# Performance work log

Measured on AMD Instinct MI355X. Metric: run time of the kernel, lower is better.

Reference implementation:

```python
import jax, jax.numpy as jnp
import numpy as np
from jax import lax

D_MODEL = 512
CLASS_NUM = 8000
MAX_LEN = 80
VOCAB = 8002  # len(char2idx): chars + sos/eos
SOS_IDX = 0


def setup_inputs() -> dict:
    key = jax.random.key(0)
    ks = jax.random.split(key, 16)
    T, B, D, V, C = 128, 128, D_MODEL, VOCAB, CLASS_NUM
    s = 1.0 / np.sqrt(D)
    inp = {
        "inputs": jax.random.normal(ks[0], (T, B, D), jnp.float32),
        # additive attention params (query_size=key_size=hidden_size=D)
        "Wq": jax.random.normal(ks[1], (D, D), jnp.float32) * s,
        "bq": jnp.zeros((D,), jnp.float32),
        "Wk": jax.random.normal(ks[2], (D, D), jnp.float32) * s,
        "bk": jnp.zeros((D,), jnp.float32),
        "v": jax.random.normal(ks[3], (D,), jnp.float32) * s,
        # GRUCell: input_size = 2*D, hidden_size = D (PyTorch layout)
        "W_ih": jax.random.normal(ks[4], (3 * D, 2 * D), jnp.float32) * s,
        "b_ih": jnp.zeros((3 * D,), jnp.float32),
        "W_hh": jax.random.normal(ks[5], (3 * D, D), jnp.float32) * s,
        "b_hh": jnp.zeros((3 * D,), jnp.float32),
        # embedding table and classifier
        "emb": jax.random.normal(ks[6], (V, D), jnp.float32),
        "Wc": jax.random.normal(ks[7], (C, D), jnp.float32) * s,
        "bc": jnp.zeros((C,), jnp.float32),
    }
    return inp


def _gru_cell(x, h, W_ih, b_ih, W_hh, b_hh):
    # PyTorch GRUCell math
    gi = x @ W_ih.T + b_ih  # [B, 3D]
    gh = h @ W_hh.T + b_hh  # [B, 3D]
    i_r, i_z, i_n = jnp.split(gi, 3, axis=1)
    h_r, h_z, h_n = jnp.split(gh, 3, axis=1)
    r = jax.nn.sigmoid(i_r + h_r)
    z = jax.nn.sigmoid(i_z + h_z)
    n = jnp.tanh(i_n + r * h_n)
    return (1.0 - z) * n + z * h


def reference(inputs, Wq, bq, Wk, bk, v, W_ih, b_ih, W_hh, b_hh, emb, Wc, bc):
    T, B, D = inputs.shape
    # Attention is called as attention(inputs, keys) with keys = inputs each
    # step -> weights are loop-invariant; compute the context once.
    e = jnp.tanh(inputs @ Wq.T + bq + inputs @ Wk.T + bk) @ v  # [T, B]
    att = jax.nn.softmax(e, axis=0)[..., None]  # [T, B, 1]
    c = jnp.sum(att * inputs, axis=0)  # [B, D]

    h0 = inputs[0]  # initial GRU hidden = first encoder frame
    out0 = emb[jnp.full((B,), SOS_IDX, dtype=jnp.int32)]  # sos embedding

    def step(carry, _):
        h, out = carry
        x = jnp.concatenate([out, c], axis=1)  # [B, 2D]
        h = _gru_cell(x, h, W_ih, b_ih, W_hh, b_hh)
        pred = h @ Wc.T + bc  # [B, class_num]
        top1 = jnp.argmax(pred, axis=1)  # greedy decode (eval mode)
        return (h, emb[top1]), pred

    _, preds = lax.scan(step, (h0, out0), None, length=MAX_LEN)
    return preds  # [max_len, B, class_num]
```

## Files before the change

### kernel.cpp

```cpp
#include <hip/hip_runtime.h>
#include <cstdint>
#include <cstddef>

#define D_MOD 512
#define TH3   1536
#define CLS   8000
#define MAXLEN 80
#define B_SZ  128
#define T_LEN 128
#define NK0   16
#define EGI_ROWS 8000

typedef __attribute__((ext_vector_type(8))) __bf16 bf16x8;
typedef __attribute__((ext_vector_type(8))) unsigned short u16x8;
typedef __attribute__((ext_vector_type(4))) float f32x4;

__device__ __forceinline__ unsigned short f2bf(float x) {
    unsigned u = __float_as_uint(x);
    unsigned r = ((u >> 16) & 1u) + 0x7fffu;
    return (unsigned short)((u + r) >> 16);
}
__device__ __forceinline__ float bf2f(unsigned short h) {
    return __uint_as_float(((unsigned)h) << 16);
}
__device__ __forceinline__ f32x4 mfma16(u16x8 a, u16x8 b, f32x4 c) {
    return __builtin_amdgcn_mfma_f32_16x16x32_bf16(
        __builtin_bit_cast(bf16x8, a), __builtin_bit_cast(bf16x8, b), c, 0, 0, 0);
}
__device__ __forceinline__ void conv8(const float* __restrict__ p, u16x8& hi, u16x8& lo) {
    float4 f0 = *(const float4*)p;
    float4 f1 = *(const float4*)(p + 4);
    float fs[8] = {f0.x, f0.y, f0.z, f0.w, f1.x, f1.y, f1.z, f1.w};
    #pragma unroll
    for (int j = 0; j < 8; ++j) {
        unsigned short h = f2bf(fs[j]);
        hi[j] = h;
        lo[j] = f2bf(fs[j] - bf2f(h));
    }
}
__device__ __forceinline__ unsigned long long packkey(float v, int n) {
    unsigned u = __float_as_uint(v);
    u = (u & 0x80000000u) ? ~u : (u | 0x80000000u);
    return ((unsigned long long)u << 32) | (unsigned)(~(unsigned)n);
}
__device__ __forceinline__ unsigned long long shfl_xor_u64(unsigned long long x, int mask) {
    unsigned lo = (unsigned)x, hi = (unsigned)(x >> 32);
    lo = __shfl_xor(lo, mask, 16);
    hi = __shfl_xor(hi, mask, 16);
    return ((unsigned long long)hi << 32) | lo;
}
__device__ __forceinline__ size_t pk_off(int n, int k) {
    int tile = n >> 4, lr = n & 15, k0i = k >> 5, lk = (k >> 3) & 3, e = k & 7;
    return ((size_t)(tile * NK0 + k0i) * 64 + (lk * 16 + lr)) * 8 + e;
}

__global__ __launch_bounds__(256) void cvt2p_kernel(
    const float* __restrict__ s1, const float* __restrict__ s2, int ld,
    long total4, unsigned short* __restrict__ hi, unsigned short* __restrict__ lo)
{
    long i4 = (long)blockIdx.x * 256 + threadIdx.x;
    if (i4 >= total4) return;
    long r = i4 >> 7;
    int c = (int)(i4 & 127) * 4;
    float4 a = *(const float4*)(s1 + r * (long)ld + c);
    if (s2) {
        float4 b = *(const float4*)(s2 + r * (long)ld + c);
        a.x += b.x; a.y += b.y; a.z += b.z; a.w += b.w;
    }
    float xs[4] = {a.x, a.y, a.z, a.w};
    unsigned short hs[4], ls[4];
    #pragma unroll
    for (int j = 0; j < 4; ++j) {
        hs[j] = f2bf(xs[j]);
        ls[j] = f2bf(xs[j] - bf2f(hs[j]));
    }
    size_t o = pk_off((int)r, c);
    *(ushort4*)(hi + o) = make_ushort4(hs[0], hs[1], hs[2], hs[3]);
    *(ushort4*)(lo + o) = make_ushort4(ls[0], ls[1], ls[2], ls[3]);
}

template<bool GATHER_CONV, bool CONVB, bool ADD2D, bool ARGMAX, int NS, int KS>
__device__ __forceinline__ void gemm_ks2(
    float* __restrict__ red,
    const unsigned short* __restrict__ Ahi, const unsigned short* __restrict__ Alo,
    const float* __restrict__ Afp, const unsigned long long* __restrict__ gslot,
    const unsigned short* __restrict__ Bhi, const unsigned short* __restrict__ Blo,
    const float* __restrict__ Bfp,
    const float* __restrict__ bias, const float* __restrict__ D2,
    float* __restrict__ C, int ldc,
    unsigned long long* __restrict__ aslot, int bx, int by)
{
    static_assert(NS * KS == 8, "8 waves per block");
    const int tid = threadIdx.x;
    const int w = tid >> 6, lane = tid & 63;
    const int lr = lane & 15, lk = lane >> 4;
    const int ns = w % NS, ks = w / NS;
    const int m0 = by * 16;
    const int n0 = (bx * NS + ns) * 32;
    const int tA = by;
    const int tB0 = n0 >> 4, tB1 = tB0 + 1;

    const float* paf = nullptr;
    if constexpr (GATHER_CONV) {
        int g = gslot ? (int)(~(unsigned)gslot[m0 + lr]) : (m0 + lr);
        paf = Afp + (size_t)g * D_MOD + lk * 8;
    }
    const float *pb0f = nullptr, *pb1f = nullptr;
    if constexpr (CONVB) {
        pb0f = Bfp + (size_t)(n0 + lr) * D_MOD + lk * 8;
        pb1f = Bfp + (size_t)(n0 + 16 + lr) * D_MOD + lk * 8;
    }

    f32x4 acc0 = (f32x4){0.f, 0.f, 0.f, 0.f};
    f32x4 acc1 = (f32x4){0.f, 0.f, 0.f, 0.f};

    const int kBeg = ks * (NK0 / KS), kEnd = kBeg + (NK0 / KS);
    for (int k0i = kBeg; k0i < kEnd; ++k0i) {
        u16x8 ah, al, b0h, b0l, b1h, b1l;
        if constexpr (GATHER_CONV) {
            conv8(paf + k0i * 32, ah, al);
        } else {
            size_t oA = ((size_t)(tA * NK0 + k0i) * 64 + lane) * 8;
            ah = *(const u16x8*)(Ahi + oA); al = *(const u16x8*)(Alo + oA);
        }
        if constexpr (CONVB) {
            conv8(pb0f + k0i * 32, b0h, b0l);
            conv8(pb1f + k0i * 32, b1h, b1l);
        } else {
            size_t oB0 = ((size_t)(tB0 * NK0 + k0i) * 64 + lane) * 8;
            size_t oB1 = ((size_t)(tB1 * NK0 + k0i) * 64 + lane) * 8;
            b0h = *(const u16x8*)(Bhi + oB0); b0l = *(const u16x8*)(Blo + oB0);
            b1h = *(const u16x8*)(Bhi + oB1); b1l = *(const u16x8*)(Blo + oB1);
        }
        acc0 = mfma16(ah, b0h, acc0);
        acc0 = mfma16(ah, b0l, acc0);
        acc0 = mfma16(al, b0h, acc0);
        acc1 = mfma16(ah, b1h, acc1);
        acc1 = mfma16(ah, b1l, acc1);
        acc1 = mfma16(al, b1h, acc1);
    }

    float af[8];
    #pragma unroll
    for (int i = 0; i < 4; ++i) { af[i] = acc0[i]; af[4 + i] = acc1[i]; }

    if (ks > 0) {
        const int slot = (ks - 1) * NS + ns;
        #pragma unroll
        for (int i = 0; i < 8; ++i) red[slot * 576 + lane * 9 + i] = af[i];
    }
    __syncthreads();
    if (ks == 0) {
        #pragma unroll
        for (int j = 1; j < KS; ++j) {
            const int slot = (j - 1) * NS + ns;
            #pragma unroll
            for (int i = 0; i < 8; ++i) af[i] += red[slot * 576 + lane * 9 + i];
        }
        #pragma unroll
        for (int r = 0; r < 4; ++r) {
            const int row = m0 + lk * 4 + r;
            unsigned long long kmax = 0ull;
            #pragma unroll
            for (int ni = 0; ni < 2; ++ni) {
                const int col = n0 + ni * 16 + lr;
                float val = af[ni * 4 + r];
                if (bias) val += bias[col];
                if constexpr (ADD2D) val += D2[(size_t)row * ldc + col];
                C[(size_t)row * ldc + col] = val;
                if constexpr (ARGMAX) {
                    unsigned long long k = packkey(val, col);
                    if (k > kmax) kmax = k;
                }
            }
            if constexpr (ARGMAX) {
                #pragma unroll
                for (int off = 1; off < 16; off <<= 1) {
                    unsigned long long o = shfl_xor_u64(kmax, off);
                    if (o > kmax) kmax = o;
                }
                if (lr == 0) atomicMax(&aslot[row], kmax);
            }
        }
    }
}

template<int G>
__device__ __forceinline__ bool xcd_map(int p, int& bx, int& by) {
    int x = p & 7, s = p >> 3;
    by = s & 7;
    bx = x * G + (s >> 3);
    return true;
}

__global__ __launch_bounds__(512) void egi_kernel(
    const float* __restrict__ emb,
    const unsigned short* __restrict__ WihaHi, const unsigned short* __restrict__ WihaLo,
    float* __restrict__ Egi)
{
    __shared__ float red[7 * 576];
    int p = blockIdx.x;
    int x = p & 7, s = p >> 3;
    int by = s % 500, bx = x * 6 + s / 500;
    gemm_ks2<true, false, false, false, 1, 8>(red, nullptr, nullptr, emb, nullptr,
        WihaHi, WihaLo, nullptr, nullptr, nullptr, Egi, TH3, nullptr, bx, by);
}

__global__ __launch_bounds__(512) void gh_kernel(
    const unsigned short* __restrict__ hHi, const unsigned short* __restrict__ hLo,
    const unsigned short* __restrict__ WhhHi, const unsigned short* __restrict__ WhhLo,
    const float* __restrict__ b_hh, float* __restrict__ gh)
{
    __shared__ float red[7 * 576];
    int bx, by;
    xcd_map<6>(blockIdx.x, bx, by);
    gemm_ks2<false, false, false, false, 1, 8>(red, hHi, hLo, nullptr, nullptr,
        WhhHi, WhhLo, nullptr, b_hh, nullptr, gh, TH3, nullptr, bx, by);
}

template<bool CONVB>
__global__ __launch_bounds__(512) void cls_gh_kernel(
    const unsigned short* __restrict__ hHi, const unsigned short* __restrict__ hLo,
    const unsigned short* __restrict__ WcHi, const unsigned short* __restrict__ WcLo,
    const float* __restrict__ Wc, const float* __restrict__ bc,
    float* __restrict__ C, unsigned long long* __restrict__ aslot,
    const unsigned short* __restrict__ WhhHi, const unsigned short* __restrict__ WhhLo,
    const float* __restrict__ b_hh, float* __restrict__ gh)
{
    __shared__ float red[7 * 576];
    const int p = blockIdx.x;
    if (p < 1024) {
        int bx, by;
        xcd_map<16>(p, bx, by);
        if (bx >= 125) return;
        gemm_ks2<false, CONVB, false, true, 2, 4>(red, hHi, hLo, nullptr, nullptr,
            WcHi, WcLo, Wc, bc, nullptr, C, CLS, aslot, bx, by);
    } else {
        int bx, by;
        xcd_map<6>(p - 1024, bx, by);
        gemm_ks2<false, false, false, false, 1, 8>(red, hHi, hLo, nullptr, nullptr,
            WhhHi, WhhLo, nullptr, b_hh, nullptr, gh, TH3, nullptr, bx, by);
    }
}

__global__ __launch_bounds__(512) void step_dual_kernel(
    const unsigned short* __restrict__ hHi, const unsigned short* __restrict__ hLo,
    const unsigned short* __restrict__ WhhHi, const unsigned short* __restrict__ WhhLo,
    const float* __restrict__ b_hh,
    const float* __restrict__ emb, const unsigned long long* __restrict__ sPrev,
    const unsigned short* __restrict__ WihaHi, const unsigned short* __restrict__ WihaLo,
    const float* __restrict__ gc,
    float* __restrict__ gh, float* __restrict__ gi)
{
    __shared__ float red[7 * 576];
    int p = blockIdx.x;
    const int z = (p >= 384);
    p -= z * 384;
    int bx, by;
    xcd_map<6>(p, bx, by);
    if (z == 0)
        gemm_ks2<false, false, false, false, 1, 8>(red, hHi, hLo, nullptr, nullptr,
            WhhHi, WhhLo, nullptr, b_hh, nullptr, gh, TH3, nullptr, bx, by);
    else
        gemm_ks2<true, false, true, false, 1, 8>(red, nullptr, nullptr, emb, sPrev,
            WihaHi, WihaLo, nullptr, nullptr, gc, gi, TH3, nullptr, bx, by);
}

__global__ __launch_bounds__(512) void gemm128_kernel(
    const unsigned short* __restrict__ Ahi, const unsigned short* __restrict__ Alo,
    const unsigned short* __restrict__ Bhi, const unsigned short* __restrict__ Blo,
    const float* __restrict__ bias, float* __restrict__ C)
{
    __shared__ float red[7 * 576];
    int bx, by;
    xcd_map<6>(blockIdx.x, bx, by);
    gemm_ks2<false, false, false, false, 1, 8>(red, Ahi, Alo, nullptr, nullptr,
        Bhi, Blo, nullptr, bias, nullptr, C, TH3, nullptr, bx, by);
}

template<bool CONVB>
__global__ __launch_bounds__(512) void cls_kernel(
    const unsigned short* __restrict__ hHi, const unsigned short* __restrict__ hLo,
    const unsigned short* __restrict__ WcHi, const unsigned short* __restrict__ WcLo,
    const float* __restrict__ Wc, const float* __restrict__ bc,
    float* __restrict__ C, unsigned long long* __restrict__ aslot)
{
    __shared__ float red[3 * 2 * 576];
    int bx, by;
    xcd_map<16>(blockIdx.x, bx, by);
    if (bx >= 125) return;
    gemm_ks2<false, CONVB, false, true, 2, 4>(red, hHi, hLo, nullptr, nullptr,
        WcHi, WcLo, Wc, bc, nullptr, C, CLS, aslot, bx, by);
}

__global__ __launch_bounds__(256) void attn_e_mfma(
    const float* __restrict__ inp,
    const unsigned short* __restrict__ WqkHi, const unsigned short* __restrict__ WqkLo,
    const float* __restrict__ bq, const float* __restrict__ bk,
    const float* __restrict__ v, float* __restrict__ e)
{
    __shared__ __align__(16) unsigned short Ah[32][40];
    __shared__ __align__(16) unsigned short Al[32][40];
    __shared__ float red[4][32];
    const int tid = threadIdx.x, w = tid >> 6, lane = tid & 63;
    const int lr = lane & 15, lk = lane >> 4;
    const int m0 = blockIdx.x * 32;
    const int srow = tid >> 3, scol = (tid & 7) * 4;

    f32x4 acc[2][8];
    #pragma unroll
    for (int i = 0; i < 2; ++i)
        #pragma unroll
        for (int j = 0; j < 8; ++j) acc[i][j] = (f32x4){0.f, 0.f, 0.f, 0.f};

    for (int k0i = 0; k0i < NK0; ++k0i) {
        float4 x = *(const float4*)(inp + (size_t)(m0 + srow) * D_MOD + k0i * 32 + scol);
        float xs[4] = {x.x, x.y, x.z, x.w};
        #pragma unroll
        for (int j = 0; j < 4; ++j) {
            unsigned short h = f2bf(xs[j]);
            Ah[srow][scol + j] = h;
            Al[srow][scol + j] = f2bf(xs[j] - bf2f(h));
        }
        __syncthreads();
        u16x8 a[2][2];
        #pragma unroll
        for (int mi = 0; mi < 2; ++mi) {
            a[mi][0] = *(const u16x8*)&Ah[mi * 16 + lr][lk * 8];
            a[mi][1] = *(const u16x8*)&Al[mi * 16 + lr][lk * 8];
        }
        #pragma unroll
        for (int nf = 0; nf < 8; ++nf) {
            const int tile = w * 8 + nf;
            size_t ob = ((size_t)(tile * NK0 + k0i) * 64 + lane) * 8;
            u16x8 bh = *(const u16x8*)(WqkHi + ob);
            u16x8 bl = *(const u16x8*)(WqkLo + ob);
            #pragma unroll
            for (int mi = 0; mi < 2; ++mi) {
                acc[mi][nf] = mfma16(a[mi][0], bh, acc[mi][nf]);
                acc[mi][nf] = mfma16(a[mi][0], bl, acc[mi][nf]);
                acc[mi][nf] = mfma16(a[mi][1], bh, acc[mi][nf]);
            }
        }
        __syncthreads();
    }

    float ep[2][4];
    #pragma unroll
    for (int mi = 0; mi < 2; ++mi)
        #pragma unroll
        for (int r = 0; r < 4; ++r) ep[mi][r] = 0.f;
    #pragma unroll
    for (int nf = 0; nf < 8; ++nf) {
        const int col = w * 128 + nf * 16 + lr;
        const float bb = bq[col] + bk[col];
        const float vv = v[col];
        #pragma unroll
        for (int mi = 0; mi < 2; ++mi)
            #pragma unroll
            for (int r = 0; r < 4; ++r)
                ep[mi][r] += vv * tanhf(acc[mi][nf][r] + bb);
    }
    #pragma unroll
    for (int mi = 0; mi < 2; ++mi)
        #pragma unroll
        for (int r = 0; r < 4; ++r) {
            float s = ep[mi][r];
            #pragma unroll
            for (int off = 1; off < 16; off <<= 1) s += __shfl_xor(s, off, 16);
            if (lr == 0) red[w][mi * 16 + lk * 4 + r] = s;
        }
    __syncthreads();
    if (tid < 32) e[m0 + tid] = red[0][tid] + red[1][tid] + red[2][tid] + red[3][tid];
}

__global__ __launch_bounds__(256) void softmax_ctx_kernel(
    const float* __restrict__ inp, const float* __restrict__ e,
    unsigned short* __restrict__ cHi, unsigned short* __restrict__ cLo,
    float* __restrict__ h1, unsigned short* __restrict__ h1Hi, unsigned short* __restrict__ h1Lo,
    unsigned long long* __restrict__ slots)
{
    __shared__ float att[T_LEN];
    __shared__ float red;
    const int b = blockIdx.x, tid = threadIdx.x;
    float val = -1e30f;
    if (tid < T_LEN) { val = e[(size_t)tid * B_SZ + b]; att[tid] = val; }
    __syncthreads();
    if (tid < 64) {
        float m = fmaxf(att[tid], att[tid + 64]);
        #pragma unroll
        for (int off = 32; off; off >>= 1) m = fmaxf(m, __shfl_xor(m, off));
        if (tid == 0) red = m;
    }
    __syncthreads();
    const float mx = red;
    __syncthreads();
    if (tid < T_LEN) att[tid] = expf(val - mx);
    __syncthreads();
    if (tid < 64) {
        float s = att[tid] + att[tid + 64];
        #pragma unroll
        for (int off = 32; off; off >>= 1) s += __shfl_xor(s, off);
        if (tid == 0) red = s;
    }
    __syncthreads();
    const float inv = 1.f / red;

    const int d0 = tid * 2;
    float ax = 0.f, ay = 0.f;
    for (int t = 0; t < T_LEN; ++t) {
        float a = att[t];
        float2 x = *(const float2*)(inp + ((size_t)t * B_SZ + b) * D_MOD + d0);
        ax += a * x.x; ay += a * x.y;
        if (t == 0) {
            *(float2*)(h1 + (size_t)b * D_MOD + d0) = x;
            unsigned short hx = f2bf(x.x), hy = f2bf(x.y);
            h1Hi[pk_off(b, d0)]     = hx;
            h1Hi[pk_off(b, d0 + 1)] = hy;
            h1Lo[pk_off(b, d0)]     = f2bf(x.x - bf2f(hx));
            h1Lo[pk_off(b, d0 + 1)] = f2bf(x.y - bf2f(hy));
        }
    }
    ax *= inv; ay *= inv;
    unsigned short cx = f2bf(ax), cy = f2bf(ay);
    cHi[pk_off(b, d0)]     = cx;
    cHi[pk_off(b, d0 + 1)] = cy;
    cLo[pk_off(b, d0)]     = f2bf(ax - bf2f(cx));
    cLo[pk_off(b, d0 + 1)] = f2bf(ay - bf2f(cy));
    if (tid == 0) {
        slots[b] = 0ull;
        slots[B_SZ + b] = 0x00000000FFFFFFFFull;
    }
}

__global__ __launch_bounds__(512) void gru_combine(
    const float* __restrict__ gh, const float* __restrict__ gi,
    const float* __restrict__ hPrev, float* __restrict__ hCur,
    unsigned short* __restrict__ hHiC, unsigned short* __restrict__ hLoC,
    unsigned long long* __restrict__ slotCur)
{
    const int b = blockIdx.x, k = threadIdx.x;
    const float* gib = gi + (size_t)b * TH3;
    const float* ghb = gh + (size_t)b * TH3;
    float r = 1.f / (1.f + expf(-(gib[k] + ghb[k])));
    float z = 1.f / (1.f + expf(-(gib[k + 512] + ghb[k + 512])));
    float n = tanhf(gib[k + 1024] + r * ghb[k + 1024]);
    float h = hPrev[(size_t)b * D_MOD + k];
    float hv = (1.f - z) * n + z * h;
    hCur[(size_t)b * D_MOD + k] = hv;
    unsigned short hh = f2bf(hv);
    size_t o = pk_off(b, k);
    hHiC[o] = hh;
    hLoC[o] = f2bf(hv - bf2f(hh));
    if (k == 0) slotCur[b] = 0ull;
}

__global__ __launch_bounds__(512) void gru_combine_egi(
    const float* __restrict__ gh, const float* __restrict__ Egi,
    const float* __restrict__ gc, const unsigned long long* __restrict__ sPrev,
    const float* __restrict__ hPrev, float* __restrict__ hCur,
    unsigned short* __restrict__ hHiC, unsigned short* __restrict__ hLoC,
    unsigned long long* __restrict__ slotCur)
{
    const int b = blockIdx.x, k = threadIdx.x;
    const int sel = (int)(~(unsigned)sPrev[b]);
    const float* gib = Egi + (size_t)sel * TH3;
    const float* gcb = gc + (size_t)b * TH3;
    const float* ghb = gh + (size_t)b * TH3;
    float gi0 = gib[k] + gcb[k];
    float gi1 = gib[k + 512] + gcb[k + 512];
    float gi2 = gib[k + 1024] + gcb[k + 1024];
    float r = 1.f / (1.f + expf(-(gi0 + ghb[k])));
    float z = 1.f / (1.f + expf(-(gi1 + ghb[k + 512])));
    float n = tanhf(gi2 + r * ghb[k + 1024]);
    float h = hPrev[(size_t)b * D_MOD + k];
    float hv = (1.f - z) * n + z * h;
    hCur[(size_t)b * D_MOD + k] = hv;
    unsigned short hh = f2bf(hv);
    size_t o = pk_off(b, k);
    hHiC[o] = hh;
    hLoC[o] = f2bf(hv - bf2f(hh));
    if (k == 0) slotCur[b] = 0ull;
}

extern "C" void kernel_launch(void* const* d_in, const int* in_sizes, int n_in,
                              void* d_out, int out_size, void* d_ws, size_t ws_size,
                              hipStream_t stream)
{
    const float* inp  = (const float*)d_in[0];
    const float* Wq   = (const float*)d_in[1];
    const float* bq   = (const float*)d_in[2];
    const float* Wk   = (const float*)d_in[3];
    const float* bk   = (const float*)d_in[4];
    const float* v    = (const float*)d_in[5];
    const float* W_ih = (const float*)d_in[6];
    const float* b_ih = (const float*)d_in[7];
    const float* W_hh = (const float*)d_in[8];
    const float* b_hh = (const float*)d_in[9];
    const float* emb  = (const float*)d_in[10];
    const float* Wc   = (const float*)d_in[11];
    const float* bc   = (const float*)d_in[12];
    float* out = (float*)d_out;

    char* base = (char*)d_ws;
    size_t off = 0;
    auto alloc = [&](size_t bytes) -> char* {
        char* q = base + off;
        off += (bytes + 255) & ~(size_t)255;
        return q;
    };
    typedef unsigned short us;
    us* WqkHi  = (us*)alloc(512 * 512 * 2);
    us* WqkLo  = (us*)alloc(512 * 512 * 2);
    us* WhhHi  = (us*)alloc((size_t)TH3 * 512 * 2);
    us* WhhLo  = (us*)alloc((size_t)TH3 * 512 * 2);
    us* WihaHi = (us*)alloc((size_t)TH3 * 512 * 2);
    us* WihaLo = (us*)alloc((size_t)TH3 * 512 * 2);
    us* WihbHi = (us*)alloc((size_t)TH3 * 512 * 2);
    us* WihbLo = (us*)alloc((size_t)TH3 * 512 * 2);
    float* e   = (float*)alloc(T_LEN * B_SZ * 4);
    us* cHi    = (us*)alloc(B_SZ * 512 * 2);
    us* cLo    = (us*)alloc(B_SZ * 512 * 2);
    float* gc  = (float*)alloc((size_t)B_SZ * TH3 * 4);
    float* gh  = (float*)alloc((size_t)B_SZ * TH3 * 4);
    float* gi  = (float*)alloc((size_t)B_SZ * TH3 * 4);
    float* hF[2]; us* hHi[2]; us* hLo[2];
    hF[0] = (float*)alloc(B_SZ * 512 * 4);
    hF[1] = (float*)alloc(B_SZ * 512 * 4);
    hHi[0] = (us*)alloc(B_SZ * 512 * 2);
    hHi[1] = (us*)alloc(B_SZ * 512 * 2);
    hLo[0] = (us*)alloc(B_SZ * 512 * 2);
    hLo[1] = (us*)alloc(B_SZ * 512 * 2);
    unsigned long long* slots = (unsigned long long*)alloc(2 * B_SZ * 8);
    us* WcHi = (us*)alloc((size_t)CLS * 512 * 2);
    us* WcLo = (us*)alloc((size_t)CLS * 512 * 2);
    const bool PREB = (off <= ws_size);
    float* Egi = (float*)alloc((size_t)EGI_ROWS * TH3 * 4);
    const bool EGIB = (off <= ws_size);

    cvt2p_kernel<<<(512 * 128) / 256, 256, 0, stream>>>(Wq, Wk, 512, 512L * 128, WqkHi, WqkLo);
    cvt2p_kernel<<<(TH3 * 128) / 256, 256, 0, stream>>>(W_hh, nullptr, 512, (long)TH3 * 128, WhhHi, WhhLo);
    cvt2p_kernel<<<(TH3 * 128) / 256, 256, 0, stream>>>(W_ih, nullptr, 1024, (long)TH3 * 128, WihaHi, WihaLo);
    cvt2p_kernel<<<(TH3 * 128) / 256, 256, 0, stream>>>(W_ih + 512, nullptr, 1024, (long)TH3 * 128, WihbHi, WihbLo);
    if (PREB)
        cvt2p_kernel<<<(CLS * 128) / 256, 256, 0, stream>>>(Wc, nullptr, 512, (long)CLS * 128, WcHi, WcLo);
    if (EGIB)
        egi_kernel<<<8 * 6 * 500, 512, 0, stream>>>(emb, WihaHi, WihaLo, Egi);

    attn_e_mfma<<<(T_LEN * B_SZ) / 32, 256, 0, stream>>>(inp, WqkHi, WqkLo, bq, bk, v, e);
    softmax_ctx_kernel<<<B_SZ, 256, 0, stream>>>(inp, e, cHi, cLo, hF[1], hHi[1], hLo[1], slots);
    gemm128_kernel<<<384, 512, 0, stream>>>(cHi, cLo, WihbHi, WihbLo, b_ih, gc);

    if (EGIB) {
        gh_kernel<<<384, 512, 0, stream>>>(hHi[1], hLo[1], WhhHi, WhhLo, b_hh, gh);
        for (int t = 0; t < MAXLEN; ++t) {
            const int pi = (t + 1) & 1, ci = t & 1;
            unsigned long long* sPrev = slots + pi * B_SZ;
            unsigned long long* sCur  = slots + ci * B_SZ;

            gru_combine_egi<<<B_SZ, 512, 0, stream>>>(
                gh, Egi, gc, sPrev, hF[pi], hF[ci], hHi[ci], hLo[ci], sCur);
            if (PREB)
                cls_gh_kernel<false><<<1408, 512, 0, stream>>>(
                    hHi[ci], hLo[ci], WcHi, WcLo, nullptr, bc,
                    out + (size_t)t * B_SZ * CLS, sCur,
                    WhhHi, WhhLo, b_hh, gh);
            else
                cls_gh_kernel<true><<<1408, 512, 0, stream>>>(
                    hHi[ci], hLo[ci], nullptr, nullptr, Wc, bc,
                    out + (size_t)t * B_SZ * CLS, sCur,
                    WhhHi, WhhLo, b_hh, gh);
        }
    } else {
        for (int t = 0; t < MAXLEN; ++t) {
            const int pi = (t + 1) & 1, ci = t & 1;
            unsigned long long* sPrev = slots + pi * B_SZ;
            unsigned long long* sCur  = slots + ci * B_SZ;

            step_dual_kernel<<<768, 512, 0, stream>>>(
                hHi[pi], hLo[pi], WhhHi, WhhLo, b_hh,
                emb, sPrev, WihaHi, WihaLo, gc, gh, gi);
            gru_combine<<<B_SZ, 512, 0, stream>>>(
                gh, gi, hF[pi], hF[ci], hHi[ci], hLo[ci], sCur);
            if (PREB)
                cls_kernel<false><<<1024, 512, 0, stream>>>(
                    hHi[ci], hLo[ci], WcHi, WcLo, nullptr, bc,
                    out + (size_t)t * B_SZ * CLS, sCur);
            else
                cls_kernel<true><<<1024, 512, 0, stream>>>(
                    hHi[ci], hLo[ci], nullptr, nullptr, Wc, bc,
                    out + (size_t)t * B_SZ * CLS, sCur);
        }
    }
}
```

Baseline: 2.615 ms.

## Fuse GRU combine into classifier step kernel with in-grid atomic barrier

```diff
diff --git a/kernel.cpp b/kernel.cpp
--- a/kernel.cpp
+++ b/kernel.cpp
@@ -10,6 +10,7 @@
 #define T_LEN 128
 #define NK0   16
 #define EGI_ROWS 8000
+#define CTR_WORDS (MAXLEN * 32)
 
 typedef __attribute__((ext_vector_type(8))) __bf16 bf16x8;
 typedef __attribute__((ext_vector_type(8))) unsigned short u16x8;
@@ -79,7 +80,8 @@
     *(ushort4*)(lo + o) = make_ushort4(ls[0], ls[1], ls[2], ls[3]);
 }
 
-template<bool GATHER_CONV, bool CONVB, bool ADD2D, bool ARGMAX, int NS, int KS>
+template<bool GATHER_CONV, bool CONVB, bool ADD2D, bool ARGMAX, bool NT, bool ATOMA,
+         int NS, int KS>
 __device__ __forceinline__ void gemm_ks2(
     float* __restrict__ red,
     const unsigned short* __restrict__ Ahi, const unsigned short* __restrict__ Alo,
@@ -119,6 +121,18 @@
         u16x8 ah, al, b0h, b0l, b1h, b1l;
         if constexpr (GATHER_CONV) {
             conv8(paf + k0i * 32, ah, al);
+        } else if constexpr (ATOMA) {
+            size_t oA = ((size_t)(tA * NK0 + k0i) * 64 + lane) * 8;
+            const unsigned long long* pa =
+                reinterpret_cast<const unsigned long long*>(Ahi + oA);
+            const unsigned long long* pl =
+                reinterpret_cast<const unsigned long long*>(Alo + oA);
+            union { unsigned long long q[2]; u16x8 v; } ua, ul;
+            ua.q[0] = __hip_atomic_load(pa, __ATOMIC_RELAXED, __HIP_MEMORY_SCOPE_AGENT);
+            ua.q[1] = __hip_atomic_load(pa + 1, __ATOMIC_RELAXED, __HIP_MEMORY_SCOPE_AGENT);
+            ul.q[0] = __hip_atomic_load(pl, __ATOMIC_RELAXED, __HIP_MEMORY_SCOPE_AGENT);
+            ul.q[1] = __hip_atomic_load(pl + 1, __ATOMIC_RELAXED, __HIP_MEMORY_SCOPE_AGENT);
+            ah = ua.v; al = ul.v;
         } else {
             size_t oA = ((size_t)(tA * NK0 + k0i) * 64 + lane) * 8;
             ah = *(const u16x8*)(Ahi + oA); al = *(const u16x8*)(Alo + oA);
@@ -167,7 +181,8 @@
                 float val = af[ni * 4 + r];
                 if (bias) val += bias[col];
                 if constexpr (ADD2D) val += D2[(size_t)row * ldc + col];
-                C[(size_t)row * ldc + col] = val;
+                if constexpr (NT) __builtin_nontemporal_store(val, &C[(size_t)row * ldc + col]);
+                else C[(size_t)row * ldc + col] = val;
                 if constexpr (ARGMAX) {
                     unsigned long long k = packkey(val, col);
                     if (k > kmax) kmax = k;
@@ -193,276 +208,14 @@
     return true;
 }
 
-__global__ __launch_bounds__(512) void egi_kernel(
-    const float* __restrict__ emb,
-    const unsigned short* __restrict__ WihaHi, const unsigned short* __restrict__ WihaLo,
-    float* __restrict__ Egi)
-{
-    __shared__ float red[7 * 576];
-    int p = blockIdx.x;
-    int x = p & 7, s = p >> 3;
-    int by = s % 500, bx = x * 6 + s / 500;
-    gemm_ks2<true, false, false, false, 1, 8>(red, nullptr, nullptr, emb, nullptr,
-        WihaHi, WihaLo, nullptr, nullptr, nullptr, Egi, TH3, nullptr, bx, by);
-}
-
-__global__ __launch_bounds__(512) void gh_kernel(
-    const unsigned short* __restrict__ hHi, const unsigned short* __restrict__ hLo,
-    const unsigned short* __restrict__ WhhHi, const unsigned short* __restrict__ WhhLo,
-    const float* __restrict__ b_hh, float* __restrict__ gh)
-{
-    __shared__ float red[7 * 576];
-    int bx, by;
-    xcd_map<6>(blockIdx.x, bx, by);
-    gemm_ks2<false, false, false, false, 1, 8>(red, hHi, hLo, nullptr, nullptr,
-        WhhHi, WhhLo, nullptr, b_hh, nullptr, gh, TH3, nullptr, bx, by);
-}
-
-template<bool CONVB>
-__global__ __launch_bounds__(512) void cls_gh_kernel(
-    const unsigned short* __restrict__ hHi, const unsigned short* __restrict__ hLo,
-    const unsigned short* __restrict__ WcHi, const unsigned short* __restrict__ WcLo,
-    const float* __restrict__ Wc, const float* __restrict__ bc,
-    float* __restrict__ C, unsigned long long* __restrict__ aslot,
-    const unsigned short* __restrict__ WhhHi, const unsigned short* __restrict__ WhhLo,
-    const float* __restrict__ b_hh, float* __restrict__ gh)
-{
-    __shared__ float red[7 * 576];
-    const int p = blockIdx.x;
-    if (p < 1024) {
-        int bx, by;
-        xcd_map<16>(p, bx, by);
-        if (bx >= 125) return;
-        gemm_ks2<false, CONVB, false, true, 2, 4>(red, hHi, hLo, nullptr, nullptr,
-            WcHi, WcLo, Wc, bc, nullptr, C, CLS, aslot, bx, by);
-    } else {
-        int bx, by;
-        xcd_map<6>(p - 1024, bx, by);
-        gemm_ks2<false, false, false, false, 1, 8>(red, hHi, hLo, nullptr, nullptr,
-            WhhHi, WhhLo, nullptr, b_hh, nullptr, gh, TH3, nullptr, bx, by);
-    }
-}
-
-__global__ __launch_bounds__(512) void step_dual_kernel(
-    const unsigned short* __restrict__ hHi, const unsigned short* __restrict__ hLo,
-    const unsigned short* __restrict__ WhhHi, const unsigned short* __restrict__ WhhLo,
-    const float* __restrict__ b_hh,
-    const float* __restrict__ emb, const unsigned long long* __restrict__ sPrev,
-    const unsigned short* __restrict__ WihaHi, const unsigned short* __restrict__ WihaLo,
-    const float* __restrict__ gc,
-    float* __restrict__ gh, float* __restrict__ gi)
-{
-    __shared__ float red[7 * 576];
-    int p = blockIdx.x;
-    const int z = (p >= 384);
-    p -= z * 384;
-    int bx, by;
-    xcd_map<6>(p, bx, by);
-    if (z == 0)
-        gemm_ks2<false, false, false, false, 1, 8>(red, hHi, hLo, nullptr, nullptr,
-            WhhHi, WhhLo, nullptr, b_hh, nullptr, gh, TH3, nullptr, bx, by);
-    else
-        gemm_ks2<true, false, true, false, 1, 8>(red, nullptr, nullptr, emb, sPrev,
-            WihaHi, WihaLo, nullptr, nullptr, gc, gi, TH3, nullptr, bx, by);
-}
-
-__global__ __launch_bounds__(512) void gemm128_kernel(
-    const unsigned short* __restrict__ Ahi, const unsigned short* __restrict__ Alo,
-    const unsigned short* __restrict__ Bhi, const unsigned short* __restrict__ Blo,
-    const float* __restrict__ bias, float* __restrict__ C)
-{
-    __shared__ float red[7 * 576];
-    int bx, by;
-    xcd_map<6>(blockIdx.x, bx, by);
-    gemm_ks2<false, false, false, false, 1, 8>(red, Ahi, Alo, nullptr, nullptr,
-        Bhi, Blo, nullptr, bias, nullptr, C, TH3, nullptr, bx, by);
-}
-
-template<bool CONVB>
-__global__ __launch_bounds__(512) void cls_kernel(
-    const unsigned short* __restrict__ hHi, const unsigned short* __restrict__ hLo,
-    const unsigned short* __restrict__ WcHi, const unsigned short* __restrict__ WcLo,
-    const float* __restrict__ Wc, const float* __restrict__ bc,
-    float* __restrict__ C, unsigned long long* __restrict__ aslot)
-{
-    __shared__ float red[3 * 2 * 576];
-    int bx, by;
-    xcd_map<16>(blockIdx.x, bx, by);
-    if (bx >= 125) return;
-    gemm_ks2<false, CONVB, false, true, 2, 4>(red, hHi, hLo, nullptr, nullptr,
-        WcHi, WcLo, Wc, bc, nullptr, C, CLS, aslot, bx, by);
-}
-
-__global__ __launch_bounds__(256) void attn_e_mfma(
-    const float* __restrict__ inp,
-    const unsigned short* __restrict__ WqkHi, const unsigned short* __restrict__ WqkLo,
-    const float* __restrict__ bq, const float* __restrict__ bk,
-    const float* __restrict__ v, float* __restrict__ e)
-{
-    __shared__ __align__(16) unsigned short Ah[32][40];
-    __shared__ __align__(16) unsigned short Al[32][40];
-    __shared__ float red[4][32];
-    const int tid = threadIdx.x, w = tid >> 6, lane = tid & 63;
-    const int lr = lane & 15, lk = lane >> 4;
-    const int m0 = blockIdx.x * 32;
-    const int srow = tid >> 3, scol = (tid & 7) * 4;
-
-    f32x4 acc[2][8];
-    #pragma unroll
-    for (int i = 0; i < 2; ++i)
-        #pragma unroll
-        for (int j = 0; j < 8; ++j) acc[i][j] = (f32x4){0.f, 0.f, 0.f, 0.f};
-
-    for (int k0i = 0; k0i < NK0; ++k0i) {
-        float4 x = *(const float4*)(inp + (size_t)(m0 + srow) * D_MOD + k0i * 32 + scol);
-        float xs[4] = {x.x, x.y, x.z, x.w};
-        #pragma unroll
-        for (int j = 0; j < 4; ++j) {
-            unsigned short h = f2bf(xs[j]);
-            Ah[srow][scol + j] = h;
-            Al[srow][scol + j] = f2bf(xs[j] - bf2f(h));
-        }
-        __syncthreads();
-        u16x8 a[2][2];
-        #pragma unroll
-        for (int mi = 0; mi < 2; ++mi) {
-            a[mi][0] = *(const u16x8*)&Ah[mi * 16 + lr][lk * 8];
-            a[mi][1] = *(const u16x8*)&Al[mi * 16 + lr][lk * 8];
-        }
-        #pragma unroll
-        for (int nf = 0; nf < 8; ++nf) {
-            const int tile = w * 8 + nf;
-            size_t ob = ((size_t)(tile * NK0 + k0i) * 64 + lane) * 8;
-            u16x8 bh = *(const u16x8*)(WqkHi + ob);
-            u16x8 bl = *(const u16x8*)(WqkLo + ob);
-            #pragma unroll
-            for (int mi = 0; mi < 2; ++mi) {
-                acc[mi][nf] = mfma16(a[mi][0], bh, acc[mi][nf]);
-                acc[mi][nf] = mfma16(a[mi][0], bl, acc[mi][nf]);
-                acc[mi][nf] = mfma16(a[mi][1], bh, acc[mi][nf]);
-            }
-        }
-        __syncthreads();
-    }
-
-    float ep[2][4];
-    #pragma unroll
-    for (int mi = 0; mi < 2; ++mi)
-        #pragma unroll
-        for (int r = 0; r < 4; ++r) ep[mi][r] = 0.f;
-    #pragma unroll
-    for (int nf = 0; nf < 8; ++nf) {
-        const int col = w * 128 + nf * 16 + lr;
-        const float bb = bq[col] + bk[col];
-        const float vv = v[col];
-        #pragma unroll
-        for (int mi = 0; mi < 2; ++mi)
-            #pragma unroll
-            for (int r = 0; r < 4; ++r)
-                ep[mi][r] += vv * tanhf(acc[mi][nf][r] + bb);
-    }
-    #pragma unroll
-    for (int mi = 0; mi < 2; ++mi)
-        #pragma unroll
-        for (int r = 0; r < 4; ++r) {
-            float s = ep[mi][r];
-            #pragma unroll
-            for (int off = 1; off < 16; off <<= 1) s += __shfl_xor(s, off, 16);
-            if (lr == 0) red[w][mi * 16 + lk * 4 + r] = s;
-        }
-    __syncthreads();
-    if (tid < 32) e[m0 + tid] = red[0][tid] + red[1][tid] + red[2][tid] + red[3][tid];
-}
-
-__global__ __launch_bounds__(256) void softmax_ctx_kernel(
-    const float* __restrict__ inp, const float* __restrict__ e,
-    unsigned short* __restrict__ cHi, unsigned short* __restrict__ cLo,
-    float* __restrict__ h1, unsigned short* __restrict__ h1Hi, unsigned short* __restrict__ h1Lo,
-    unsigned long long* __restrict__ slots)
-{
-    __shared__ float att[T_LEN];
-    __shared__ float red;
-    const int b = blockIdx.x, tid = threadIdx.x;
-    float val = -1e30f;
-    if (tid < T_LEN) { val = e[(size_t)tid * B_SZ + b]; att[tid] = val; }
-    __syncthreads();
-    if (tid < 64) {
-        float m = fmaxf(att[tid], att[tid + 64]);
-        #pragma unroll
-        for (int off = 32; off; off >>= 1) m = fmaxf(m, __shfl_xor(m, off));
-        if (tid == 0) red = m;
-    }
-    __syncthreads();
-    const float mx = red;
-    __syncthreads();
-    if (tid < T_LEN) att[tid] = expf(val - mx);
-    __syncthreads();
-    if (tid < 64) {
-        float s = att[tid] + att[tid + 64];
-        #pragma unroll
-        for (int off = 32; off; off >>= 1) s += __shfl_xor(s, off);
-        if (tid == 0) red = s;
-    }
-    __syncthreads();
-    const float inv = 1.f / red;
-
-    const int d0 = tid * 2;
-    float ax = 0.f, ay = 0.f;
-    for (int t = 0; t < T_LEN; ++t) {
-        float a = att[t];
-        float2 x = *(const float2*)(inp + ((size_t)t * B_SZ + b) * D_MOD + d0);
-        ax += a * x.x; ay += a * x.y;
-        if (t == 0) {
-            *(float2*)(h1 + (size_t)b * D_MOD + d0) = x;
-            unsigned short hx = f2bf(x.x), hy = f2bf(x.y);
-            h1Hi[pk_off(b, d0)]     = hx;
-            h1Hi[pk_off(b, d0 + 1)] = hy;
-            h1Lo[pk_off(b, d0)]     = f2bf(x.x - bf2f(hx));
-            h1Lo[pk_off(b, d0 + 1)] = f2bf(x.y - bf2f(hy));
-        }
-    }
-    ax *= inv; ay *= inv;
-    unsigned short cx = f2bf(ax), cy = f2bf(ay);
-    cHi[pk_off(b, d0)]     = cx;
-    cHi[pk_off(b, d0 + 1)] = cy;
-    cLo[pk_off(b, d0)]     = f2bf(ax - bf2f(cx));
-    cLo[pk_off(b, d0 + 1)] = f2bf(ay - bf2f(cy));
-    if (tid == 0) {
-        slots[b] = 0ull;
-        slots[B_SZ + b] = 0x00000000FFFFFFFFull;
-    }
-}
-
-__global__ __launch_bounds__(512) void gru_combine(
-    const float* __restrict__ gh, const float* __restrict__ gi,
-    const float* __restrict__ hPrev, float* __restrict__ hCur,
-    unsigned short* __restrict__ hHiC, unsigned short* __restrict__ hLoC,
-    unsigned long long* __restrict__ slotCur)
-{
-    const int b = blockIdx.x, k = threadIdx.x;
-    const float* gib = gi + (size_t)b * TH3;
-    const float* ghb = gh + (size_t)b * TH3;
-    float r = 1.f / (1.f + expf(-(gib[k] + ghb[k])));
-    float z = 1.f / (1.f + expf(-(gib[k + 512] + ghb[k + 512])));
-    float n = tanhf(gib[k + 1024] + r * ghb[k + 1024]);
-    float h = hPrev[(size_t)b * D_MOD + k];
-    float hv = (1.f - z) * n + z * h;
-    hCur[(size_t)b * D_MOD + k] = hv;
-    unsigned short hh = f2bf(hv);
-    size_t o = pk_off(b, k);
-    hHiC[o] = hh;
-    hLoC[o] = f2bf(hv - bf2f(hh));
-    if (k == 0) slotCur[b] = 0ull;
-}
-
-__global__ __launch_bounds__(512) void gru_combine_egi(
-    const float* __restrict__ gh, const float* __restrict__ Egi,
+__device__ __forceinline__ void gru_job_egi(
+    int b, const float* __restrict__ gh, const float* __restrict__ Egi,
     const float* __restrict__ gc, const unsigned long long* __restrict__ sPrev,
     const float* __restrict__ hPrev, float* __restrict__ hCur,
     unsigned short* __restrict__ hHiC, unsigned short* __restrict__ hLoC,
     unsigned long long* __restrict__ slotCur)
 {
-    const int b = blockIdx.x, k = threadIdx.x;
+    const int k = threadIdx.x;
     const int sel = (int)(~(unsigned)sPrev[b]);
     const float* gib = Egi + (size_t)sel * TH3;
     const float* gcb = gc + (size_t)b * TH3;
@@ -481,6 +234,363 @@
     hHiC[o] = hh;
     hLoC[o] = f2bf(hv - bf2f(hh));
     if (k == 0) slotCur[b] = 0ull;
+}
+
+__global__ __launch_bounds__(512) void fused_step_kernel(
+    const unsigned short* __restrict__ WhhHi, const unsigned short* __restrict__ WhhLo,
+    const float* __restrict__ b_hh,
+    const unsigned short* __restrict__ WcHi, const unsigned short* __restrict__ WcLo,
+    const float* __restrict__ bc,
+    const float* __restrict__ Egi, const float* __restrict__ gc,
+    float* __restrict__ gh,
+    const unsigned long long* __restrict__ sPrev, unsigned long long* __restrict__ sCur,
+    const float* __restrict__ hPrevF, float* __restrict__ hCurF,
+    unsigned short* __restrict__ hHiC, unsigned short* __restrict__ hLoC,
+    float* __restrict__ out, unsigned* __restrict__ ctr)
+{
+    __shared__ float red[7 * 576];
+    __shared__ unsigned tk_sh;
+    const int tid = threadIdx.x;
+    unsigned* done = ctr + 16;
+
+    if (tid == 0)
+        tk_sh = __hip_atomic_fetch_add(ctr, 1u, __ATOMIC_RELAXED, __HIP_MEMORY_SCOPE_AGENT);
+    __syncthreads();
+    const unsigned tk = tk_sh;
+
+    if (tk < (unsigned)B_SZ) {
+        const int b = (int)tk, k = tid;
+        const int sel = (int)(~(unsigned)sPrev[b]);
+        const float* gib = Egi + (size_t)sel * TH3;
+        const float* gcb = gc + (size_t)b * TH3;
+        const float* ghb = gh + (size_t)b * TH3;
+        float gi0 = gib[k] + gcb[k];
+        float gi1 = gib[k + 512] + gcb[k + 512];
+        float gi2 = gib[k + 1024] + gcb[k + 1024];
+        float r = 1.f / (1.f + expf(-(gi0 + ghb[k])));
+        float z = 1.f / (1.f + expf(-(gi1 + ghb[k + 512])));
+        float n = tanhf(gi2 + r * ghb[k + 1024]);
+        float h = hPrevF[(size_t)b * D_MOD + k];
+        float hv = (1.f - z) * n + z * h;
+        hCurF[(size_t)b * D_MOD + k] = hv;
+        unsigned short hh = f2bf(hv);
+        unsigned short ll = f2bf(hv - bf2f(hh));
+        unsigned hh_u = hh, ll_u = ll;
+        unsigned hh_n = __shfl_down(hh_u, 1);
+        unsigned ll_n = __shfl_down(ll_u, 1);
+        if ((k & 1) == 0) {
+            size_t o = pk_off(b, k);
+            __hip_atomic_store((unsigned*)(hHiC + o), hh_u | (hh_n << 16),
+                               __ATOMIC_RELAXED, __HIP_MEMORY_SCOPE_AGENT);
+            __hip_atomic_store((unsigned*)(hLoC + o), ll_u | (ll_n << 16),
+                               __ATOMIC_RELAXED, __HIP_MEMORY_SCOPE_AGENT);
+        }
+        if (k == 0)
+            __hip_atomic_store(&sCur[b], 0ull, __ATOMIC_RELAXED, __HIP_MEMORY_SCOPE_AGENT);
+        __syncthreads();
+        if (tid == 0) {
+            asm volatile("s_waitcnt vmcnt(0)" ::: "memory");
+            __hip_atomic_fetch_add(done, 1u, __ATOMIC_RELAXED, __HIP_MEMORY_SCOPE_AGENT);
+        }
+    }
+
+    if (tid == 0) {
+        while (__hip_atomic_load(done, __ATOMIC_RELAXED, __HIP_MEMORY_SCOPE_AGENT)
+               < (unsigned)B_SZ)
+            __builtin_amdgcn_s_sleep(4);
+    }
+    __syncthreads();
+    asm volatile("" ::: "memory");
+
+    const int p = (int)blockIdx.x;
+    if (p < 1024) {
+        int bx, by;
+        xcd_map<16>(p, bx, by);
+        if (bx < 125)
+            gemm_ks2<false, false, false, true, true, true, 2, 4>(red,
+                hHiC, hLoC, nullptr, nullptr, WcHi, WcLo, nullptr, bc, nullptr,
+                out, CLS, sCur, bx, by);
+    } else {
+        int bx, by;
+        xcd_map<6>(p - 1024, bx, by);
+        gemm_ks2<false, false, false, false, false, true, 1, 8>(red,
+            hHiC, hLoC, nullptr, nullptr, WhhHi, WhhLo, nullptr, b_hh, nullptr,
+            gh, TH3, nullptr, bx, by);
+    }
+}
+
+__global__ __launch_bounds__(512) void egi_kernel(
+    const float* __restrict__ emb,
+    const unsigned short* __restrict__ WihaHi, const unsigned short* __restrict__ WihaLo,
+    float* __restrict__ Egi)
+{
+    __shared__ float red[7 * 576];
+    int p = blockIdx.x;
+    int x = p & 7, s = p >> 3;
+    int by = s % 500, bx = x * 6 + s / 500;
+    gemm_ks2<true, false, false, false, false, false, 1, 8>(red, nullptr, nullptr,
+        emb, nullptr, WihaHi, WihaLo, nullptr, nullptr, nullptr, Egi, TH3, nullptr, bx, by);
+}
+
+__global__ __launch_bounds__(512) void gh_kernel(
+    const unsigned short* __restrict__ hHi, const unsigned short* __restrict__ hLo,
+    const unsigned short* __restrict__ WhhHi, const unsigned short* __restrict__ WhhLo,
+    const float* __restrict__ b_hh, float* __restrict__ gh)
+{
+    __shared__ float red[7 * 576];
+    int bx, by;
+    xcd_map<6>(blockIdx.x, bx, by);
+    gemm_ks2<false, false, false, false, false, false, 1, 8>(red, hHi, hLo, nullptr, nullptr,
+        WhhHi, WhhLo, nullptr, b_hh, nullptr, gh, TH3, nullptr, bx, by);
+}
+
+template<bool CONVB>
+__global__ __launch_bounds__(512) void cls_gh_kernel(
+    const unsigned short* __restrict__ hHi, const unsigned short* __restrict__ hLo,
+    const unsigned short* __restrict__ WcHi, const unsigned short* __restrict__ WcLo,
+    const float* __restrict__ Wc, const float* __restrict__ bc,
+    float* __restrict__ C, unsigned long long* __restrict__ aslot,
+    const unsigned short* __restrict__ WhhHi, const unsigned short* __restrict__ WhhLo,
+    const float* __restrict__ b_hh, float* __restrict__ gh)
+{
+    __shared__ float red[7 * 576];
+    const int p = blockIdx.x;
+    if (p < 1024) {
+        int bx, by;
+        xcd_map<16>(p, bx, by);
+        if (bx >= 125) return;
+        gemm_ks2<false, CONVB, false, true, false, false, 2, 4>(red, hHi, hLo, nullptr, nullptr,
+            WcHi, WcLo, Wc, bc, nullptr, C, CLS, aslot, bx, by);
+    } else {
+        int bx, by;
+        xcd_map<6>(p - 1024, bx, by);
+        gemm_ks2<false, false, false, false, false, false, 1, 8>(red, hHi, hLo, nullptr, nullptr,
+            WhhHi, WhhLo, nullptr, b_hh, nullptr, gh, TH3, nullptr, bx, by);
+    }
+}
+
+__global__ __launch_bounds__(512) void step_dual_kernel(
+    const unsigned short* __restrict__ hHi, const unsigned short* __restrict__ hLo,
+    const unsigned short* __restrict__ WhhHi, const unsigned short* __restrict__ WhhLo,
+    const float* __restrict__ b_hh,
+    const float* __restrict__ emb, const unsigned long long* __restrict__ sPrev,
+    const unsigned short* __restrict__ WihaHi, const unsigned short* __restrict__ WihaLo,
+    const float* __restrict__ gc,
+    float* __restrict__ gh, float* __restrict__ gi)
+{
+    __shared__ float red[7 * 576];
+    int p = blockIdx.x;
+    const int z = (p >= 384);
+    p -= z * 384;
+    int bx, by;
+    xcd_map<6>(p, bx, by);
+    if (z == 0)
+        gemm_ks2<false, false, false, false, false, false, 1, 8>(red, hHi, hLo, nullptr, nullptr,
+            WhhHi, WhhLo, nullptr, b_hh, nullptr, gh, TH3, nullptr, bx, by);
+    else
+        gemm_ks2<true, false, true, false, false, false, 1, 8>(red, nullptr, nullptr, emb, sPrev,
+            WihaHi, WihaLo, nullptr, nullptr, gc, gi, TH3, nullptr, bx, by);
+}
+
+__global__ __launch_bounds__(512) void gemm128_kernel(
+    const unsigned short* __restrict__ Ahi, const unsigned short* __restrict__ Alo,
+    const unsigned short* __restrict__ Bhi, const unsigned short* __restrict__ Blo,
+    const float* __restrict__ bias, float* __restrict__ C)
+{
+    __shared__ float red[7 * 576];
+    int bx, by;
+    xcd_map<6>(blockIdx.x, bx, by);
+    gemm_ks2<false, false, false, false, false, false, 1, 8>(red, Ahi, Alo, nullptr, nullptr,
+        Bhi, Blo, nullptr, bias, nullptr, C, TH3, nullptr, bx, by);
+}
+
+template<bool CONVB>
+__global__ __launch_bounds__(512) void cls_kernel(
+    const unsigned short* __restrict__ hHi, const unsigned short* __restrict__ hLo,
+    const unsigned short* __restrict__ WcHi, const unsigned short* __restrict__ WcLo,
+    const float* __restrict__ Wc, const float* __restrict__ bc,
+    float* __restrict__ C, unsigned long long* __restrict__ aslot)
+{
+    __shared__ float red[3 * 2 * 576];
+    int bx, by;
+    xcd_map<16>(blockIdx.x, bx, by);
+    if (bx >= 125) return;
+    gemm_ks2<false, CONVB, false, true, false, false, 2, 4>(red, hHi, hLo, nullptr, nullptr,
+        WcHi, WcLo, Wc, bc, nullptr, C, CLS, aslot, bx, by);
+}
+
+__global__ __launch_bounds__(256) void attn_e_mfma(
+    const float* __restrict__ inp,
+    const unsigned short* __restrict__ WqkHi, const unsigned short* __restrict__ WqkLo,
+    const float* __restrict__ bq, const float* __restrict__ bk,
+    const float* __restrict__ v, float* __restrict__ e)
+{
+    __shared__ __align__(16) unsigned short Ah[32][40];
+    __shared__ __align__(16) unsigned short Al[32][40];
+    __shared__ float red[4][32];
+    const int tid = threadIdx.x, w = tid >> 6, lane = tid & 63;
+    const int lr = lane & 15, lk = lane >> 4;
+    const int m0 = blockIdx.x * 32;
+    const int srow = tid >> 3, scol = (tid & 7) * 4;
+
+    f32x4 acc[2][8];
+    #pragma unroll
+    for (int i = 0; i < 2; ++i)
+        #pragma unroll
+        for (int j = 0; j < 8; ++j) acc[i][j] = (f32x4){0.f, 0.f, 0.f, 0.f};
+
+    for (int k0i = 0; k0i < NK0; ++k0i) {
+        float4 x = *(const float4*)(inp + (size_t)(m0 + srow) * D_MOD + k0i * 32 + scol);
+        float xs[4] = {x.x, x.y, x.z, x.w};
+        #pragma unroll
+        for (int j = 0; j < 4; ++j) {
+            unsigned short h = f2bf(xs[j]);
+            Ah[srow][scol + j] = h;
+            Al[srow][scol + j] = f2bf(xs[j] - bf2f(h));
+        }
+        __syncthreads();
+        u16x8 a[2][2];
+        #pragma unroll
+        for (int mi = 0; mi < 2; ++mi) {
+            a[mi][0] = *(const u16x8*)&Ah[mi * 16 + lr][lk * 8];
+            a[mi][1] = *(const u16x8*)&Al[mi * 16 + lr][lk * 8];
+        }
+        #pragma unroll
+        for (int nf = 0; nf < 8; ++nf) {
+            const int tile = w * 8 + nf;
+            size_t ob = ((size_t)(tile * NK0 + k0i) * 64 + lane) * 8;
+            u16x8 bh = *(const u16x8*)(WqkHi + ob);
+            u16x8 bl = *(const u16x8*)(WqkLo + ob);
+            #pragma unroll
+            for (int mi = 0; mi < 2; ++mi) {
+                acc[mi][nf] = mfma16(a[mi][0], bh, acc[mi][nf]);
+                acc[mi][nf] = mfma16(a[mi][0], bl, acc[mi][nf]);
+                acc[mi][nf] = mfma16(a[mi][1], bh, acc[mi][nf]);
+            }
+        }
+        __syncthreads();
+    }
+
+    float ep[2][4];
+    #pragma unroll
+    for (int mi = 0; mi < 2; ++mi)
+        #pragma unroll
+        for (int r = 0; r < 4; ++r) ep[mi][r] = 0.f;
+    #pragma unroll
+    for (int nf = 0; nf < 8; ++nf) {
+        const int col = w * 128 + nf * 16 + lr;
+        const float bb = bq[col] + bk[col];
+        const float vv = v[col];
+        #pragma unroll
+        for (int mi = 0; mi < 2; ++mi)
+            #pragma unroll
+            for (int r = 0; r < 4; ++r)
+                ep[mi][r] += vv * tanhf(acc[mi][nf][r] + bb);
+    }
+    #pragma unroll
+    for (int mi = 0; mi < 2; ++mi)
+        #pragma unroll
+        for (int r = 0; r < 4; ++r) {
+            float s = ep[mi][r];
+            #pragma unroll
+            for (int off = 1; off < 16; off <<= 1) s += __shfl_xor(s, off, 16);
+            if (lr == 0) red[w][mi * 16 + lk * 4 + r] = s;
+        }
+    __syncthreads();
+    if (tid < 32) e[m0 + tid] = red[0][tid] + red[1][tid] + red[2][tid] + red[3][tid];
+}
+
+__global__ __launch_bounds__(256) void softmax_ctx_kernel(
+    const float* __restrict__ inp, const float* __restrict__ e,
+    unsigned short* __restrict__ cHi, unsigned short* __restrict__ cLo,
+    float* __restrict__ h1, unsigned short* __restrict__ h1Hi, unsigned short* __restrict__ h1Lo,
+    unsigned long long* __restrict__ slots, unsigned* __restrict__ ctrs)
+{
+    __shared__ float att[T_LEN];
+    __shared__ float red;
+    const int b = blockIdx.x, tid = threadIdx.x;
+    if (b == 0)
+        for (int i = tid; i < CTR_WORDS; i += 256) ctrs[i] = 0u;
+    float val = -1e30f;
+    if (tid < T_LEN) { val = e[(size_t)tid * B_SZ + b]; att[tid] = val; }
+    __syncthreads();
+    if (tid < 64) {
+        float m = fmaxf(att[tid], att[tid + 64]);
+        #pragma unroll
+        for (int off = 32; off; off >>= 1) m = fmaxf(m, __shfl_xor(m, off));
+        if (tid == 0) red = m;
+    }
+    __syncthreads();
+    const float mx = red;
+    __syncthreads();
+    if (tid < T_LEN) att[tid] = expf(val - mx);
+    __syncthreads();
+    if (tid < 64) {
+        float s = att[tid] + att[tid + 64];
+        #pragma unroll
+        for (int off = 32; off; off >>= 1) s += __shfl_xor(s, off);
+        if (tid == 0) red = s;
+    }
+    __syncthreads();
+    const float inv = 1.f / red;
+
+    const int d0 = tid * 2;
+    float ax = 0.f, ay = 0.f;
+    for (int t = 0; t < T_LEN; ++t) {
+        float a = att[t];
+        float2 x = *(const float2*)(inp + ((size_t)t * B_SZ + b) * D_MOD + d0);
+        ax += a * x.x; ay += a * x.y;
+        if (t == 0) {
+            *(float2*)(h1 + (size_t)b * D_MOD + d0) = x;
+            unsigned short hx = f2bf(x.x), hy = f2bf(x.y);
+            h1Hi[pk_off(b, d0)]     = hx;
+            h1Hi[pk_off(b, d0 + 1)] = hy;
+            h1Lo[pk_off(b, d0)]     = f2bf(x.x - bf2f(hx));
+            h1Lo[pk_off(b, d0 + 1)] = f2bf(x.y - bf2f(hy));
+        }
+    }
+    ax *= inv; ay *= inv;
+    unsigned short cx = f2bf(ax), cy = f2bf(ay);
+    cHi[pk_off(b, d0)]     = cx;
+    cHi[pk_off(b, d0 + 1)] = cy;
+    cLo[pk_off(b, d0)]     = f2bf(ax - bf2f(cx));
+    cLo[pk_off(b, d0 + 1)] = f2bf(ay - bf2f(cy));
+    if (tid == 0) {
+        slots[b] = 0ull;
+        slots[B_SZ + b] = 0x00000000FFFFFFFFull;
+    }
+}
+
+__global__ __launch_bounds__(512) void gru_combine(
+    const float* __restrict__ gh, const float* __restrict__ gi,
+    const float* __restrict__ hPrev, float* __restrict__ hCur,
+    unsigned short* __restrict__ hHiC, unsigned short* __restrict__ hLoC,
+    unsigned long long* __restrict__ slotCur)
+{
+    const int b = blockIdx.x, k = threadIdx.x;
+    const float* gib = gi + (size_t)b * TH3;
+    const float* ghb = gh + (size_t)b * TH3;
+    float r = 1.f / (1.f + expf(-(gib[k] + ghb[k])));
+    float z = 1.f / (1.f + expf(-(gib[k + 512] + ghb[k + 512])));
+    float n = tanhf(gib[k + 1024] + r * ghb[k + 1024]);
+    float h = hPrev[(size_t)b * D_MOD + k];
+    float hv = (1.f - z) * n + z * h;
+    hCur[(size_t)b * D_MOD + k] = hv;
+    unsigned short hh = f2bf(hv);
+    size_t o = pk_off(b, k);
+    hHiC[o] = hh;
+    hLoC[o] = f2bf(hv - bf2f(hh));
+    if (k == 0) slotCur[b] = 0ull;
+}
+
+__global__ __launch_bounds__(512) void gru_combine_egi(
+    const float* __restrict__ gh, const float* __restrict__ Egi,
+    const float* __restrict__ gc, const unsigned long long* __restrict__ sPrev,
+    const float* __restrict__ hPrev, float* __restrict__ hCur,
+    unsigned short* __restrict__ hHiC, unsigned short* __restrict__ hLoC,
+    unsigned long long* __restrict__ slotCur)
+{
+    gru_job_egi(blockIdx.x, gh, Egi, gc, sPrev, hPrev, hCur, hHiC, hLoC, slotCur);
 }
 
 extern "C" void kernel_launch(void* const* d_in, const int* in_sizes, int n_in,
@@ -532,6 +642,7 @@
     hLo[0] = (us*)alloc(B_SZ * 512 * 2);
     hLo[1] = (us*)alloc(B_SZ * 512 * 2);
     unsigned long long* slots = (unsigned long long*)alloc(2 * B_SZ * 8);
+    unsigned* ctrs = (unsigned*)alloc(CTR_WORDS * 4);
     us* WcHi = (us*)alloc((size_t)CLS * 512 * 2);
     us* WcLo = (us*)alloc((size_t)CLS * 512 * 2);
     const bool PREB = (off <= ws_size);
@@ -548,35 +659,37 @@
         egi_kernel<<<8 * 6 * 500, 512, 0, stream>>>(emb, WihaHi, WihaLo, Egi);
 
     attn_e_mfma<<<(T_LEN * B_SZ) / 32, 256, 0, stream>>>(inp, WqkHi, WqkLo, bq, bk, v, e);
-    softmax_ctx_kernel<<<B_SZ, 256, 0, stream>>>(inp, e, cHi, cLo, hF[1], hHi[1], hLo[1], slots);
+    softmax_ctx_kernel<<<B_SZ, 256, 0, stream>>>(inp, e, cHi, cLo, hF[1], hHi[1], hLo[1], slots, ctrs);
     gemm128_kernel<<<384, 512, 0, stream>>>(cHi, cLo, WihbHi, WihbLo, b_ih, gc);
 
-    if (EGIB) {
+    if (EGIB && PREB) {
+        gh_kernel<<<384, 512, 0, stream>>>(hHi[1], hLo[1], WhhHi, WhhLo, b_hh, gh);
+        for (int t = 0; t < MAXLEN; ++t) {
+            const int pi = (t + 1) & 1, ci = t & 1;
+            fused_step_kernel<<<1408, 512, 0, stream>>>(
+                WhhHi, WhhLo, b_hh, WcHi, WcLo, bc, Egi, gc, gh,
+                slots + pi * B_SZ, slots + ci * B_SZ,
+                hF[pi], hF[ci], hHi[ci], hLo[ci],
+                out + (size_t)t * B_SZ * CLS, ctrs + t * 32);
+        }
+    } else if (EGIB) {
         gh_kernel<<<384, 512, 0, stream>>>(hHi[1], hLo[1], WhhHi, WhhLo, b_hh, gh);
         for (int t = 0; t < MAXLEN; ++t) {
             const int pi = (t + 1) & 1, ci = t & 1;
             unsigned long long* sPrev = slots + pi * B_SZ;
             unsigned long long* sCur  = slots + ci * B_SZ;
-
             gru_combine_egi<<<B_SZ, 512, 0, stream>>>(
                 gh, Egi, gc, sPrev, hF[pi], hF[ci], hHi[ci], hLo[ci], sCur);
-            if (PREB)
-                cls_gh_kernel<false><<<1408, 512, 0, stream>>>(
-                    hHi[ci], hLo[ci], WcHi, WcLo, nullptr, bc,
-                    out + (size_t)t * B_SZ * CLS, sCur,
-                    WhhHi, WhhLo, b_hh, gh);
-            else
-                cls_gh_kernel<true><<<1408, 512, 0, stream>>>(
-                    hHi[ci], hLo[ci], nullptr, nullptr, Wc, bc,
-                    out + (size_t)t * B_SZ * CLS, sCur,
-                    WhhHi, WhhLo, b_hh, gh);
+            cls_gh_kernel<true><<<1408, 512, 0, stream>>>(
+                hHi[ci], hLo[ci], nullptr, nullptr, Wc, bc,
+                out + (size_t)t * B_SZ * CLS, sCur,
+                WhhHi, WhhLo, b_hh, gh);
         }
     } else {
         for (int t = 0; t < MAXLEN; ++t) {
             const int pi = (t + 1) & 1, ci = t & 1;
             unsigned long long* sPrev = slots + pi * B_SZ;
             unsigned long long* sCur  = slots + ci * B_SZ;
-
             step_dual_kernel<<<768, 512, 0, stream>>>(
                 hHi[pi], hLo[pi], WhhHi, WhhLo, b_hh,
                 emb, sPrev, WihaHi, WihaLo, gc, gh, gi);
```

Result: slower. 5.126 ms (+96.0%).
